# Optimization experiments

Measured on AMD Instinct MI355X. Metric: run time of the kernel, lower is better.

Reference implementation:

```python
import jax, jax.numpy as jnp
import numpy as np
import math

GRID = 14  # coords run 1..13 -> 13x13 spatial grid
Z = math.exp(math.log(2.0 * math.pi) + 1.0)
EPS = 1e-06

def setup_inputs() -> dict:
    key = jax.random.key(0)
    B, C = 256, 1024
    x = jax.random.normal(key, (B, GRID - 1, GRID - 1, C), dtype=jnp.float32)
    return {"feature_input": x}

def reference(feature_input) -> jnp.ndarray:
    B, H, W, C = feature_input.shape
    f = jax.nn.softmax(feature_input, axis=3)  # softmax over channel dim (dim=3)
    coords = jnp.arange(1, GRID, dtype=jnp.float32)  # [13]
    xv = coords[:, None]  # varies along spatial axis 0 (torch meshgrid 'ij')
    yv = coords[None, :]  # varies along spatial axis 1
    s = f.sum(axis=(1, 2)) + EPS  # [B, C] per-slice mass
    # soft-argmax centroids, [B, C]
    mx = (xv[None, :, :, None] * f).sum(axis=(1, 2)) / s
    my = (yv[None, :, :, None] * f).sum(axis=(1, 2)) / s
    # weighted variances, normalized by 169 and the per-slice mass
    dx2 = (xv[None, :, :, None] - mx[:, None, None, :]) ** 2
    dy2 = (yv[None, :, :, None] - my[:, None, None, :]) ** 2
    x_var = (dx2 * f).sum(axis=(1, 2)) / 169.0 / s
    y_var = (dy2 * f).sum(axis=(1, 2)) / 169.0 / s
    det_xy = (x_var + y_var) ** 2 * Z  # [B, C]
    return det_xy.sum() / B / C
```

## Files before the change

### kernel.cpp

```cpp
#include <hip/hip_runtime.h>

#ifndef __has_builtin
#define __has_builtin(x) 0
#endif

__device__ __forceinline__ float fast_exp2(float x) {
#if __has_builtin(__builtin_amdgcn_exp2f)
    return __builtin_amdgcn_exp2f(x);
#else
    return exp2f(x);
#endif
}

__device__ __forceinline__ float wave_sum_dpp(float x) {
    int v;
    v = __builtin_amdgcn_update_dpp(0, __float_as_int(x), 0x111, 0xf, 0xf, true);
    x += __int_as_float(v);
    v = __builtin_amdgcn_update_dpp(0, __float_as_int(x), 0x112, 0xf, 0xf, true);
    x += __int_as_float(v);
    v = __builtin_amdgcn_update_dpp(0, __float_as_int(x), 0x114, 0xf, 0xf, true);
    x += __int_as_float(v);
    v = __builtin_amdgcn_update_dpp(0, __float_as_int(x), 0x118, 0xf, 0xf, true);
    x += __int_as_float(v);
    v = __builtin_amdgcn_update_dpp(0, __float_as_int(x), 0x142, 0xa, 0xf, false);
    x += __int_as_float(v);
    v = __builtin_amdgcn_update_dpp(0, __float_as_int(x), 0x143, 0xc, 0xf, false);
    x += __int_as_float(v);
    return x;
}

constexpr int   kB      = 256;
constexpr int   kC      = 1024;
constexpr int   kG      = 13;
constexpr int   kP      = kG * kG;
constexpr int   kParts  = 4;
constexpr int   kMaxPP  = 43;
constexpr float kEps    = 1e-6f;
constexpr float kZ      = 17.079468445347132f;
constexpr float kLog2e  = 1.4426950408889634f;
constexpr float kInv169 = 1.0f / 169.0f;
constexpr float kScale  = 1.0f / (256.0f * 1024.0f);

__global__ __launch_bounds__(1024, 4)
void fused_kernel(const float* __restrict__ x, float* __restrict__ out)
{
    __shared__ float sP[kMaxPP * 16];
    __shared__ float sInvD[kMaxPP];
    __shared__ float sred[16];

    const int tid  = threadIdx.x;
    const int lane = tid & 63;
    const int wid  = tid >> 6;
    const int b    = blockIdx.x;

    float S0 = 0.f, S1x = 0.f, S1y = 0.f, S2x = 0.f, S2y = 0.f;

    for (int part = 0; part < kParts; ++part) {
        const int  start = part * 42;
        const bool full  = (part == 3);

        const float* __restrict__ xc =
            x + (size_t)b * kP * kC + (size_t)start * kC + tid;

        float e[kMaxPP];
        #pragma unroll
        for (int i = 0; i < kMaxPP; ++i)
            e[i] = xc[(size_t)i * kC];

        #pragma unroll
        for (int i = 0; i < kMaxPP; ++i)
            e[i] = fast_exp2(e[i] * kLog2e);

        if (!full) e[42] = 0.0f;

        #pragma unroll
        for (int i = 0; i < kMaxPP; ++i) {
            const float s = wave_sum_dpp(e[i]);
            if (lane == 63) sP[i * 16 + wid] = s;
        }
        __syncthreads();

        if (tid < kMaxPP) {
            float d = 0.f;
            #pragma unroll
            for (int w = 0; w < 16; ++w)
                d += sP[tid * 16 + w];
            sInvD[tid] = 1.0f / (d + 1e-30f);
        }
        __syncthreads();

        int h = 3 * part;
        int w = 3 * part;
        #pragma unroll
        for (int i = 0; i < kMaxPP; ++i) {
            const float f  = e[i] * sInvD[i];
            const float fx = (float)(h + 1);
            const float fy = (float)(w + 1);
            S0  += f;
            S1x  = fmaf(fx,      f, S1x);
            S1y  = fmaf(fy,      f, S1y);
            S2x  = fmaf(fx * fx, f, S2x);
            S2y  = fmaf(fy * fy, f, S2y);
            ++w;
            if (w == kG) { w = 0; ++h; }
        }
    }

    const float s   = S0 + kEps;
    const float is  = 1.0f / s;
    const float mx  = S1x * is;
    const float my  = S1y * is;
    const float nx  = S2x - mx * (2.0f * S1x - mx * S0);
    const float ny  = S2y - my * (2.0f * S1y - my * S0);
    const float t   = (nx + ny) * is * kInv169;
    float det = t * t * kZ;

    #pragma unroll
    for (int m = 1; m < 64; m <<= 1)
        det += __shfl_xor(det, m);

    if (lane == 0) sred[wid] = det;
    __syncthreads();
    if (wid == 0) {
        float v = (lane < 16) ? sred[lane] : 0.0f;
        #pragma unroll
        for (int m = 1; m < 16; m <<= 1)
            v += __shfl_xor(v, m);
        if (lane == 0) atomicAdd(out, v * kScale);
    }
}

extern "C" void kernel_launch(void* const* d_in, const int* in_sizes, int n_in,
                              void* d_out, int out_size, void* d_ws, size_t ws_size,
                              hipStream_t stream)
{
    const float* x   = (const float*)d_in[0];
    float*       out = (float*)d_out;

    hipMemsetAsync(out, 0, sizeof(float) * (size_t)out_size, stream);
    fused_kernel<<<dim3(kB), dim3(1024), 0, stream>>>(x, out);
}
```

Before: 248.6 us.

## Double-buffer spatial chunks in registers to overlap loads with softmax reductions

New measurement: 375.7 us. 1.51x slower.

```diff
diff --git a/kernel.cpp b/kernel.cpp
--- a/kernel.cpp
+++ b/kernel.cpp
@@ -29,23 +29,79 @@
     return x;
 }
 
+__device__ __forceinline__ void sync_lds() {
+    asm volatile("s_waitcnt lgkmcnt(0)" ::: "memory");
+    __builtin_amdgcn_s_barrier();
+    asm volatile("" ::: "memory");
+}
+
 constexpr int   kB      = 256;
 constexpr int   kC      = 1024;
 constexpr int   kG      = 13;
 constexpr int   kP      = kG * kG;
-constexpr int   kParts  = 4;
-constexpr int   kMaxPP  = 43;
+constexpr int   kBufP   = 22;
 constexpr float kEps    = 1e-6f;
 constexpr float kZ      = 17.079468445347132f;
 constexpr float kLog2e  = 1.4426950408889634f;
 constexpr float kInv169 = 1.0f / 169.0f;
 constexpr float kScale  = 1.0f / (256.0f * 1024.0f);
 
+template<int START, int PP, int NPP>
+__device__ __forceinline__ void do_part(
+    const float* __restrict__ xb, int tid, int lane, int wid,
+    float (&cur)[kBufP], float (&nxt)[kBufP],
+    float& S0, float& S1x, float& S1y, float& S2x, float& S2y,
+    float* __restrict__ sP, float* __restrict__ sInvD)
+{
+    if (NPP > 0) {
+        const float* __restrict__ xn = xb + (size_t)(START + PP) * kC + tid;
+        #pragma unroll
+        for (int i = 0; i < NPP; ++i)
+            nxt[i] = xn[(size_t)i * kC];
+    }
+
+    #pragma unroll
+    for (int i = 0; i < PP; ++i)
+        cur[i] = fast_exp2(cur[i] * kLog2e);
+
+    #pragma unroll
+    for (int i = 0; i < PP; ++i) {
+        const float s = wave_sum_dpp(cur[i]);
+        if (lane == 63) sP[i * 16 + wid] = s;
+    }
+    sync_lds();
+
+    if (tid < PP) {
+        float d = 0.f;
+        #pragma unroll
+        for (int w = 0; w < 16; ++w)
+            d += sP[tid * 16 + w];
+        sInvD[tid] = 1.0f / (d + 1e-30f);
+    }
+    sync_lds();
+
+    int h = START / kG;
+    int w = START - (START / kG) * kG;
+    #pragma unroll
+    for (int i = 0; i < PP; ++i) {
+        const float f  = cur[i] * sInvD[i];
+        const float fx = (float)(h + 1);
+        const float fy = (float)(w + 1);
+        S0  += f;
+        S1x  = fmaf(fx,      f, S1x);
+        S1y  = fmaf(fy,      f, S1y);
+        S2x  = fmaf(fx * fx, f, S2x);
+        S2y  = fmaf(fy * fy, f, S2y);
+        ++w;
+        if (w == kG) { w = 0; ++h; }
+    }
+}
+
 __global__ __launch_bounds__(1024, 4)
 void fused_kernel(const float* __restrict__ x, float* __restrict__ out)
 {
-    __shared__ float sP[kMaxPP * 16];
-    __shared__ float sInvD[kMaxPP];
+    __shared__ float sP[kBufP * 16];
+    __shared__ float sInvD[kBufP];
     __shared__ float sred[16];
 
     const int tid  = threadIdx.x;
@@ -53,58 +109,26 @@
     const int wid  = tid >> 6;
     const int b    = blockIdx.x;
 
+    const float* __restrict__ xb = x + (size_t)b * kP * kC;
+
+    float e0[kBufP], e1[kBufP];
     float S0 = 0.f, S1x = 0.f, S1y = 0.f, S2x = 0.f, S2y = 0.f;
 
-    for (int part = 0; part < kParts; ++part) {
-        const int  start = part * 42;
-        const bool full  = (part == 3);
+    {
+        const float* __restrict__ xc = xb + tid;
+        #pragma unroll
+        for (int i = 0; i < 21; ++i)
+            e0[i] = xc[(size_t)i * kC];
+    }
 
-        const float* __restrict__ xc =
-            x + (size_t)b * kP * kC + (size_t)start * kC + tid;
-
-        float e[kMaxPP];
-        #pragma unroll
-        for (int i = 0; i < kMaxPP; ++i)
-            e[i] = xc[(size_t)i * kC];
-
-        #pragma unroll
-        for (int i = 0; i < kMaxPP; ++i)
-            e[i] = fast_exp2(e[i] * kLog2e);
-
-        if (!full) e[42] = 0.0f;
-
-        #pragma unroll
-        for (int i = 0; i < kMaxPP; ++i) {
-            const float s = wave_sum_dpp(e[i]);
-            if (lane == 63) sP[i * 16 + wid] = s;
-        }
-        __syncthreads();
-
-        if (tid < kMaxPP) {
-            float d = 0.f;
-            #pragma unroll
-            for (int w = 0; w < 16; ++w)
-                d += sP[tid * 16 + w];
-            sInvD[tid] = 1.0f / (d + 1e-30f);
-        }
-        __syncthreads();
-
-        int h = 3 * part;
-        int w = 3 * part;
-        #pragma unroll
-        for (int i = 0; i < kMaxPP; ++i) {
-            const float f  = e[i] * sInvD[i];
-            const float fx = (float)(h + 1);
-            const float fy = (float)(w + 1);
-            S0  += f;
-            S1x  = fmaf(fx,      f, S1x);
-            S1y  = fmaf(fy,      f, S1y);
-            S2x  = fmaf(fx * fx, f, S2x);
-            S2y  = fmaf(fy * fy, f, S2y);
-            ++w;
-            if (w == kG) { w = 0; ++h; }
-        }
-    }
+    do_part<  0, 21, 21>(xb, tid, lane, wid, e0, e1, S0, S1x, S1y, S2x, S2y, sP, sInvD);
+    do_part< 21, 21, 21>(xb, tid, lane, wid, e1, e0, S0, S1x, S1y, S2x, S2y, sP, sInvD);
+    do_part< 42, 21, 21>(xb, tid, lane, wid, e0, e1, S0, S1x, S1y, S2x, S2y, sP, sInvD);
+    do_part< 63, 21, 21>(xb, tid, lane, wid, e1, e0, S0, S1x, S1y, S2x, S2y, sP, sInvD);
+    do_part< 84, 21, 21>(xb, tid, lane, wid, e0, e1, S0, S1x, S1y, S2x, S2y, sP, sInvD);
+    do_part<105, 21, 21>(xb, tid, lane, wid, e1, e0, S0, S1x, S1y, S2x, S2y, sP, sInvD);
+    do_part<126, 21, 22>(xb, tid, lane, wid, e0, e1, S0, S1x, S1y, S2x, S2y, sP, sInvD);
+    do_part<147, 22,  0>(xb, tid, lane, wid, e1, e0, S0, S1x, S1y, S2x, S2y, sP, sInvD);
 
     const float s   = S0 + kEps;
     const float is  = 1.0f / s;
```
